# Kernel optimization log

Hardware: AMD Instinct MI355X
Metric: run time of the kernel (lower is better)

## Reference

```python
import jax, jax.numpy as jnp
import numpy as np
from jax import lax


def linear_recurrence(decays, impulses):
    """s[t] = decays[t]*s[t-1] + impulses[t], s[-1]=0, via associative scan over axis 0."""
    def comb(e1, e2):
        a1, b1 = e1
        a2, b2 = e2
        return a2 * a1, a2 * b1 + b2
    return lax.associative_scan(comb, (decays, impulses), axis=0)[1]


def setup_inputs() -> dict:
    key = jax.random.key(0)
    ks = jax.random.split(key, 6)
    b, T, d = 16, 1024, 128
    n, m, k = 64, 128, 16
    x = jax.random.normal(ks[0], (b, T, d), jnp.float32)
    R = jax.random.normal(ks[1], (d, k), jnp.float32)               # fixed projection
    theta = jax.random.uniform(ks[2], (k, n // 2), jnp.float32, -np.pi, np.pi)  # eig angles
    C = jax.random.uniform(ks[3], (k, m, n), jnp.float32, -1e-6, 1e-6) / n
    D = jax.random.uniform(ks[4], (k, m), jnp.float32, -1e-3, 1e-3)
    Do = jax.random.uniform(ks[5], (m,), jnp.float32, -1e-7, 1e-7)
    return {"x": x, "R": R, "theta": theta, "C": C, "D": D, "Do": Do}


def _ldstack(x, R, theta, C, D, Do, Delta=2, standard=True):
    c64 = jnp.complex64
    b, T, d = x.shape
    k, half = theta.shape
    n = 2 * half
    m = C.shape[1]
    # (b,T,d) -> (T,b,d) complex, project d -> k
    xc = jnp.transpose(x, (1, 0, 2)).astype(c64) @ R.astype(c64)  # (T,b,k)
    # unitary eigenvalues: lnλ = i*[θ, -θ]
    lnlam = (1j * jnp.concatenate([theta, -theta], axis=1)).astype(c64)  # (k,n)
    lam = jnp.exp(lnlam)
    # B' coefficients (log-space product over eigenvalue ratios, diag excluded)
    eye = jnp.eye(n, dtype=bool)
    ratios = jnp.where(eye[None], 0.0, lam[:, :, None] / lam[:, None, :])  # (k,n,n)
    B = jnp.exp(-jnp.sum(jnp.log(1.0 - ratios), axis=1))                    # (k,n)
    # C' coefficients: C'[k,j,m] = sum_i C[k,m,i] * λ[k,j]^{-(n-i)}
    powers = (n - jnp.arange(1, n + 1)).astype(c64)           # (n,) = [n-1,...,0]
    U = jnp.exp(-powers[None, :, None] * lnlam[:, None, :])   # (k,i,j)
    Cp = jnp.einsum('kmi,kij->kjm', C.astype(c64), U)         # (k,n,m)
    Dc = D.astype(c64)
    Doc = Do.astype(c64)

    alpha = None
    y = None
    for _ in range(Delta):
        Bx = (xc[..., None] * B).reshape(T, b, k * n)          # (T,b,k*n)
        if alpha is None:
            al = jnp.broadcast_to(lam.reshape(1, 1, k * n), (T, b, k * n))
        else:
            al = (alpha * lam).reshape(T, b, k * n)
        if standard:
            z = jnp.zeros((1, b, k * n), c64)
            al = jnp.concatenate([z, al[:-1]], axis=0)
            Bx = jnp.concatenate([z, Bx[:-1]], axis=0)
        s = linear_recurrence(al, Bx).reshape(T, b, k, n)      # (T,b,k,n)
        y = (jnp.einsum('tbkn,knm->tbkm', s, Cp)
             + xc[..., None] * Dc[None, None]
             + Doc)                                            # (T,b,k,m)
        ls = lam[None, None] * s
        alpha = (1.0 / jnp.sqrt(1.0 + jnp.abs(ls) ** 2)).astype(c64)  # recipsq
    y = jnp.mean(y, axis=2).real                               # (T,b,m)
    return jnp.transpose(y, (1, 0, 2))                         # (b,T,m)


def reference(x, R, theta, C, D, Do):
    return _ldstack(x, R, theta, C, D, Do, Delta=2, standard=True)
```

## Files before the change

kernel.cpp:

```cpp
#include <hip/hip_runtime.h>
#include <math.h>

#define TLEN 1024
#define BSZ  16
#define DIN  128
#define KP   16
#define NEIG 64
#define MOUT 128
#define CHUNK_T 256
#define NCHUNK  4

static constexpr size_t XCQ_OFF = 0;
static constexpr size_t LAM_OFF = 262144;
static constexpr size_t BQ_OFF  = 264192;
static constexpr size_t CP_OFF  = 266240;
static constexpr size_t ST_OFF  = 528384;
static constexpr size_t S2_OFF  = 593920;
static constexpr size_t P_OFF   = 8982528;

__device__ __forceinline__ float f32cos(float x) { return (float)cos((double)x); }
__device__ __forceinline__ float f32sin(float x) { return (float)sin((double)x); }

__device__ __forceinline__ float2 cdiv32(float ar, float ai, float cr, float ci) {
  float2 o;
  if (fabsf(ci) <= fabsf(cr)) {
    float rat = __fdiv_rn(ci, cr);
    float scl = __fdiv_rn(1.0f, __fadd_rn(cr, __fmul_rn(ci, rat)));
    o.x = __fmul_rn(__fadd_rn(ar, __fmul_rn(ai, rat)), scl);
    o.y = __fmul_rn(__fsub_rn(ai, __fmul_rn(ar, rat)), scl);
  } else {
    float rat = __fdiv_rn(cr, ci);
    float scl = __fdiv_rn(1.0f, __fadd_rn(ci, __fmul_rn(cr, rat)));
    o.x = __fmul_rn(__fadd_rn(__fmul_rn(ar, rat), ai), scl);
    o.y = __fmul_rn(__fsub_rn(__fmul_rn(ai, rat), ar), scl);
  }
  return o;
}

__global__ __launch_bounds__(256) void k_lam_B(const float* __restrict__ theta,
                        float2* __restrict__ lam, float2* __restrict__ Bq) {
  __shared__ float2 terms[4][64];
  int wid  = threadIdx.x >> 6;
  int lane = threadIdx.x & 63;
  int idx = blockIdx.x * 4 + wid;
  int k = idx >> 6, j = idx & 63;
  float thj = (j < 32) ? theta[k * 32 + j] : -theta[k * 32 + (j - 32)];
  float ljr = f32cos(thj), lji = f32sin(thj);
  float2 tm = make_float2(0.f, 0.f);
  if (lane != j) {
    int i = lane;
    float thi = (i < 32) ? theta[k * 32 + i] : -theta[k * 32 + (i - 32)];
    float lir = f32cos(thi), lii = f32sin(thi);
    float2 r = cdiv32(lir, lii, ljr, lji);
    float tr = __fsub_rn(1.0f, r.x);
    float ti = __fsub_rn(0.0f, r.y);
    double h = sqrt((double)tr * tr + (double)ti * ti);
    tm.x = (float)log(h);
    tm.y = (float)atan2((double)ti, (double)tr);
  }
  terms[wid][lane] = tm;
  __syncthreads();
  if (lane == 0) {
    lam[idx] = make_float2(ljr, lji);
    float sr = 0.f, si = 0.f;
    for (int i = 0; i < NEIG; ++i) {
      sr = __fadd_rn(sr, terms[wid][i].x);
      si = __fadd_rn(si, terms[wid][i].y);
    }
    float er = (float)exp((double)(-sr));
    float cc = f32cos(-si), ss = f32sin(-si);
    Bq[idx] = make_float2(__fmul_rn(er, cc), __fmul_rn(er, ss));
  }
}

__global__ __launch_bounds__(128) void k_Cp(const float* __restrict__ theta,
                     const float* __restrict__ C, float2* __restrict__ Cp) {
  __shared__ float2 sU[64];
  __shared__ float  sC[128][65];
  int tid = threadIdx.x;
  int kj = blockIdx.x;
  int j = kj & 63, k = kj >> 6;
  float lnim = (j < 32) ? theta[k * 32 + j] : -theta[k * 32 + (j - 32)];
  if (tid < 64) {
    int i = tid;
    float p = (float)(63 - i);
    float ph = -__fmul_rn(p, lnim);
    sU[i] = make_float2(f32cos(ph), f32sin(ph));
  }
  const float* Ck = C + ((size_t)k << 13);
  for (int e = tid; e < 128 * 64; e += 128) {
    sC[e >> 6][e & 63] = Ck[e];
  }
  __syncthreads();
  int m = tid;
  float ar = 0.f, ai = 0.f;
  #pragma unroll 8
  for (int i = 0; i < NEIG; ++i) {
    float Cv = sC[m][i];
    float2 U = sU[i];
    ar = __fadd_rn(ar, __fmul_rn(Cv, U.x));
    ai = __fadd_rn(ai, __fmul_rn(Cv, U.y));
  }
  Cp[(size_t)(k * 64 + j) * MOUT + m] = make_float2(ar, ai);
}

__global__ __launch_bounds__(256) void k_xc(const float* __restrict__ x,
                     const float* __restrict__ R, float* __restrict__ xcq) {
  __shared__ float sX[16][132];
  __shared__ float sR[128][16];
  int tid = threadIdx.x;
  int rBase = blockIdx.x * 16;
  for (int e = tid; e < DIN * KP; e += 256) sR[e >> 4][e & 15] = R[e];
  #pragma unroll
  for (int it = 0; it < 2; ++it) {
    int e = tid + it * 256;
    int row = e >> 5, q = e & 31;
    int g = rBase + row;
    int t = g >> 4, b = g & 15;
    float4 v = *(const float4*)(x + ((size_t)b * TLEN + t) * DIN + q * 4);
    *(float4*)&sX[row][q * 4] = v;
  }
  __syncthreads();
  int r = tid >> 4, k = tid & 15;
  double acc = 0.0;
  #pragma unroll 16
  for (int d = 0; d < DIN; ++d)
    acc = fma((double)sX[r][d], (double)sR[d][k], acc);
  xcq[(size_t)(rBase + r) * KP + k] = (float)acc;
}

__global__ __launch_bounds__(64) void k_scan(const float2* __restrict__ lam,
                        const float2* __restrict__ Bq,
                        const float* __restrict__ xcq,
                        float2* __restrict__ S2,
                        float* __restrict__ state, int c) {
  __shared__ float sXq[CHUNK_T];
  int j = threadIdx.x;
  int chain = blockIdx.x;
  int b = chain >> 4, k = chain & 15;
  int mode = k * 64 + j;
  int t0 = c * CHUNK_T;
  int tlBeg = (c == 0) ? 1 : 0;
  for (int i = j; i < CHUNK_T; i += 64) {
    int g = t0 + tlBeg - 1 + i;
    sXq[i] = xcq[(size_t)g * (BSZ * KP) + b * KP + k];
  }
  __syncthreads();
  float lr = lam[mode].x, li = lam[mode].y;
  float Br = Bq[mode].x,  Bi = Bq[mode].y;
  float* st = state + (size_t)(chain * 64 + j) * 4;
  float s1r, s1i, s2r, s2i;
  if (c == 0) { s1r = s1i = s2r = s2i = 0.f; }
  else        { s1r = st[0]; s1i = st[1]; s2r = st[2]; s2i = st[3]; }
  if (c == 0)
    S2[(size_t)(0 * BSZ + b) * 1024 + mode] = make_float2(s2r, s2i);

  int tl = tlBeg;
  for (; tl + 8 <= CHUNK_T; tl += 8) {
    float als[8];
    #pragma unroll
    for (int u = 0; u < 8; ++u) {
      float xq = sXq[tl - tlBeg + u];
      float lsr = __fsub_rn(__fmul_rn(lr, s1r), __fmul_rn(li, s1i));
      float lsi = __fadd_rn(__fmul_rn(lr, s1i), __fmul_rn(li, s1r));
      float h  = (float)sqrt((double)lsr * lsr + (double)lsi * lsi);
      als[u] = __fdiv_rn(1.0f, __fsqrt_rn(__fadd_rn(1.0f, __fmul_rn(h, h))));
      float bxr = __fmul_rn(xq, Br), bxi = __fmul_rn(xq, Bi);
      s1r = __fadd_rn(lsr, bxr);
      s1i = __fadd_rn(lsi, bxi);
    }
    #pragma unroll
    for (int u = 0; u < 8; ++u) {
      float xq = sXq[tl - tlBeg + u];
      float al = als[u];
      float bxr = __fmul_rn(xq, Br), bxi = __fmul_rn(xq, Bi);
      float a2r = __fmul_rn(al, lr), a2i = __fmul_rn(al, li);
      float t2r = __fsub_rn(__fmul_rn(a2r, s2r), __fmul_rn(a2i, s2i));
      float t2i = __fadd_rn(__fmul_rn(a2r, s2i), __fmul_rn(a2i, s2r));
      s2r = __fadd_rn(t2r, bxr);
      s2i = __fadd_rn(t2i, bxi);
      S2[(size_t)((tl + u) * BSZ + b) * 1024 + mode] = make_float2(s2r, s2i);
    }
  }
  for (; tl < CHUNK_T; ++tl) {
    float xq = sXq[tl - tlBeg];
    float lsr = __fsub_rn(__fmul_rn(lr, s1r), __fmul_rn(li, s1i));
    float lsi = __fadd_rn(__fmul_rn(lr, s1i), __fmul_rn(li, s1r));
    float h  = (float)sqrt((double)lsr * lsr + (double)lsi * lsi);
    float al = __fdiv_rn(1.0f, __fsqrt_rn(__fadd_rn(1.0f, __fmul_rn(h, h))));
    float bxr = __fmul_rn(xq, Br), bxi = __fmul_rn(xq, Bi);
    float a2r = __fmul_rn(al, lr), a2i = __fmul_rn(al, li);
    float t2r = __fsub_rn(__fmul_rn(a2r, s2r), __fmul_rn(a2i, s2i));
    float t2i = __fadd_rn(__fmul_rn(a2r, s2i), __fmul_rn(a2i, s2r));
    s2r = __fadd_rn(t2r, bxr);
    s2i = __fadd_rn(t2i, bxi);
    s1r = __fadd_rn(lsr, bxr);
    s1i = __fadd_rn(lsi, bxi);
    S2[(size_t)(tl * BSZ + b) * 1024 + mode] = make_float2(s2r, s2i);
  }
  st[0] = s1r; st[1] = s1i; st[2] = s2r; st[3] = s2i;
}

__global__ __launch_bounds__(256) void k_y(const float2* __restrict__ S2,
                     const float2* __restrict__ Cp, const float* __restrict__ xcq,
                     const float* __restrict__ D, const float* __restrict__ Dov,
                     float* __restrict__ P, int c) {
  __shared__ float2 sS2t[16][65];
  __shared__ float2 sCp[16][130];
  int tid = threadIdx.x;
  int kidx = blockIdx.x >> 6;
  int rt   = blockIdx.x & 63;
  int rowBase = rt * 64;
  int rg = tid & 15;
  int cg = tid >> 4;
  int c0 = cg * 8;
  float acc[4][8];
  #pragma unroll
  for (int jj = 0; jj < 4; ++jj)
    #pragma unroll
    for (int q = 0; q < 8; ++q) acc[jj][q] = 0.f;

  #pragma unroll 1
  for (int nh = 0; nh < 4; ++nh) {
    __syncthreads();
    #pragma unroll
    for (int it = 0; it < 2; ++it) {
      int e = tid + it * 256;
      int n2 = (e & 7) * 2;
      int row = e >> 3;
      float4 v = *(const float4*)(S2 + (size_t)(rowBase + row) * 1024
                                     + kidx * 64 + nh * 16 + n2);
      sS2t[n2][row]     = make_float2(v.x, v.y);
      sS2t[n2 + 1][row] = make_float2(v.z, v.w);
    }
    #pragma unroll
    for (int it = 0; it < 4; ++it) {
      int e = tid + it * 256;
      int col2 = (e & 63) * 2;
      int n = e >> 6;
      float4 v = *(const float4*)(Cp + (size_t)(kidx * 64 + nh * 16 + n) * MOUT + col2);
      *(float4*)&sCp[n][col2] = v;
    }
    __syncthreads();
    #pragma unroll 4
    for (int n = 0; n < 16; ++n) {
      float2 a[4];
      #pragma unroll
      for (int jj = 0; jj < 4; ++jj) a[jj] = sS2t[n][rg + jj * 16];
      float4 w[4];
      #pragma unroll
      for (int q = 0; q < 4; ++q) w[q] = *(const float4*)&sCp[n][c0 + q * 2];
      float cx[8] = {w[0].x, w[0].z, w[1].x, w[1].z, w[2].x, w[2].z, w[3].x, w[3].z};
      float cy[8] = {w[0].y, w[0].w, w[1].y, w[1].w, w[2].y, w[2].w, w[3].y, w[3].w};
      #pragma unroll
      for (int jj = 0; jj < 4; ++jj)
        #pragma unroll
        for (int q = 0; q < 8; ++q)
          acc[jj][q] = __fadd_rn(acc[jj][q],
              __fsub_rn(__fmul_rn(a[jj].x, cx[q]), __fmul_rn(a[jj].y, cy[q])));
    }
  }
  float dv[8], ovv[8];
  *(float4*)&dv[0]  = *(const float4*)(D + kidx * MOUT + c0);
  *(float4*)&dv[4]  = *(const float4*)(D + kidx * MOUT + c0 + 4);
  *(float4*)&ovv[0] = *(const float4*)(Dov + c0);
  *(float4*)&ovv[4] = *(const float4*)(Dov + c0 + 4);
  #pragma unroll
  for (int jj = 0; jj < 4; ++jj) {
    int row = rowBase + rg + jj * 16;
    float xv = xcq[(size_t)(c * 4096 + row) * KP + kidx];
    float res[8];
    #pragma unroll
    for (int q = 0; q < 8; ++q)
      res[q] = __fadd_rn(__fadd_rn(acc[jj][q], __fmul_rn(xv, dv[q])), ovv[q]);
    float* pp = P + ((size_t)kidx * 4096 + row) * MOUT + c0;
    *(float4*)pp       = make_float4(res[0], res[1], res[2], res[3]);
    *(float4*)(pp + 4) = make_float4(res[4], res[5], res[6], res[7]);
  }
}

__global__ __launch_bounds__(256) void k_combine(const float* __restrict__ P,
                     float* __restrict__ out, int c) {
  int idx = blockIdx.x * 256 + threadIdx.x;
  int r  = idx >> 5;
  int m4 = (idx & 31) * 4;
  float4 s = *(const float4*)(P + (size_t)r * MOUT + m4);
  #pragma unroll
  for (int k = 1; k < KP; ++k) {
    float4 p = *(const float4*)(P + ((size_t)k * 4096 + r) * MOUT + m4);
    s.x = __fadd_rn(s.x, p.x);
    s.y = __fadd_rn(s.y, p.y);
    s.z = __fadd_rn(s.z, p.z);
    s.w = __fadd_rn(s.w, p.w);
  }
  int rg = c * 4096 + r;
  int t = rg >> 4, b = rg & 15;
  float4 res;
  res.x = __fdiv_rn(s.x, 16.0f);
  res.y = __fdiv_rn(s.y, 16.0f);
  res.z = __fdiv_rn(s.z, 16.0f);
  res.w = __fdiv_rn(s.w, 16.0f);
  *(float4*)(out + ((size_t)b * TLEN + t) * MOUT + m4) = res;
}

extern "C" void kernel_launch(void* const* d_in, const int* in_sizes, int n_in,
                              void* d_out, int out_size, void* d_ws, size_t ws_size,
                              hipStream_t stream) {
  const float* x     = (const float*)d_in[0];
  const float* R     = (const float*)d_in[1];
  const float* theta = (const float*)d_in[2];
  const float* C     = (const float*)d_in[3];
  const float* D     = (const float*)d_in[4];
  const float* Do    = (const float*)d_in[5];
  float* out = (float*)d_out;
  float* ws  = (float*)d_ws;
  float*  xcq = ws + XCQ_OFF;
  float2* lam = (float2*)(ws + LAM_OFF);
  float2* Bq  = (float2*)(ws + BQ_OFF);
  float2* Cp  = (float2*)(ws + CP_OFF);
  float*  st  = ws + ST_OFF;
  float2* S2  = (float2*)(ws + S2_OFF);
  float*  P   = ws + P_OFF;

  hipLaunchKernelGGL(k_lam_B, dim3(256),  dim3(256), 0, stream, theta, lam, Bq);
  hipLaunchKernelGGL(k_Cp,    dim3(1024), dim3(128), 0, stream, theta, C, Cp);
  hipLaunchKernelGGL(k_xc,    dim3(1024), dim3(256), 0, stream, x, R, xcq);
  for (int c = 0; c < NCHUNK; ++c) {
    hipLaunchKernelGGL(k_scan,    dim3(256),  dim3(64),  0, stream, lam, Bq, xcq, S2, st, c);
    hipLaunchKernelGGL(k_y,       dim3(1024), dim3(256), 0, stream, S2, Cp, xcq, D, Do, P, c);
    hipLaunchKernelGGL(k_combine, dim3(512),  dim3(256), 0, stream, P, out, c);
  }
}
```

Baseline: 372.1 us.

## Fuse scan, projection and combine into one software-pipelined kernel per chunk

Replaces the three per-chunk kernels with one fused kernel launched per pipeline step. Each launch runs the scan for chunk L, the C' projection for chunk L-1 and the k-reduction for chunk L-2 in separate block ranges, using double-buffered S2 and P. Chunks shrink to 128 timesteps, so there are more, smaller stages. The aim is to overlap the latency-bound serial scan, which uses only 64 blocks, with the throughput-bound GEMM and reduction, and to cut launch count. The cost is more pipeline steps and a larger branchy kernel whose register use is set by its heaviest path.

```diff
diff --git a/kernel.cpp b/kernel.cpp
--- a/kernel.cpp
+++ b/kernel.cpp
@@ -7,8 +7,9 @@
 #define KP   16
 #define NEIG 64
 #define MOUT 128
-#define CHUNK_T 256
-#define NCHUNK  4
+#define CHUNK_T 128
+#define NCHUNK  8
+#define CROWS   2048
 
 static constexpr size_t XCQ_OFF = 0;
 static constexpr size_t LAM_OFF = 262144;
@@ -129,178 +130,187 @@
   xcq[(size_t)(rBase + r) * KP + k] = (float)acc;
 }
 
-__global__ __launch_bounds__(64) void k_scan(const float2* __restrict__ lam,
-                        const float2* __restrict__ Bq,
-                        const float* __restrict__ xcq,
-                        float2* __restrict__ S2,
-                        float* __restrict__ state, int c) {
-  __shared__ float sXq[CHUNK_T];
-  int j = threadIdx.x;
-  int chain = blockIdx.x;
-  int b = chain >> 4, k = chain & 15;
-  int mode = k * 64 + j;
-  int t0 = c * CHUNK_T;
-  int tlBeg = (c == 0) ? 1 : 0;
-  for (int i = j; i < CHUNK_T; i += 64) {
-    int g = t0 + tlBeg - 1 + i;
-    sXq[i] = xcq[(size_t)g * (BSZ * KP) + b * KP + k];
-  }
-  __syncthreads();
-  float lr = lam[mode].x, li = lam[mode].y;
-  float Br = Bq[mode].x,  Bi = Bq[mode].y;
-  float* st = state + (size_t)(chain * 64 + j) * 4;
-  float s1r, s1i, s2r, s2i;
-  if (c == 0) { s1r = s1i = s2r = s2i = 0.f; }
-  else        { s1r = st[0]; s1i = st[1]; s2r = st[2]; s2i = st[3]; }
-  if (c == 0)
-    S2[(size_t)(0 * BSZ + b) * 1024 + mode] = make_float2(s2r, s2i);
-
-  int tl = tlBeg;
-  for (; tl + 8 <= CHUNK_T; tl += 8) {
-    float als[8];
+__global__ __launch_bounds__(256) void k_fused(int L,
+                     const float2* __restrict__ lam, const float2* __restrict__ Bq,
+                     const float* __restrict__ xcq, const float2* __restrict__ Cp,
+                     const float* __restrict__ D, const float* __restrict__ Dov,
+                     float2* __restrict__ S2all, float* __restrict__ Pall,
+                     float* __restrict__ state, float* __restrict__ out) {
+  __shared__ float2 sS2t[16][65];
+  __shared__ float2 sCp[16][66];
+  __shared__ float  sXq[4][132];
+  int bid = blockIdx.x;
+  int tid = threadIdx.x;
+  int nKy   = (L >= 1 && L <= 8) ? 1024 : 0;
+  int nScan = (L < 8) ? 64 : 0;
+
+  if (bid < nKy) {
+    int cK = L - 1;
+    const float2* S2 = S2all + (size_t)(cK & 1) * 2097152;
+    float* P = Pall + (size_t)(cK & 1) * 4194304;
+    int kidx = bid >> 6;
+    int rem  = bid & 63;
+    int rowBase = (rem >> 1) * 64;
+    int colBase = (rem & 1) * 64;
+    int rg = tid & 15;
+    int cg = tid >> 4;
+    float acc[4][4];
     #pragma unroll
-    for (int u = 0; u < 8; ++u) {
-      float xq = sXq[tl - tlBeg + u];
+    for (int jj = 0; jj < 4; ++jj)
+      #pragma unroll
+      for (int q = 0; q < 4; ++q) acc[jj][q] = 0.f;
+
+    #pragma unroll 1
+    for (int nh = 0; nh < 4; ++nh) {
+      __syncthreads();
+      #pragma unroll
+      for (int it = 0; it < 2; ++it) {
+        int e = tid + it * 256;
+        int n2 = (e & 7) * 2;
+        int row = e >> 3;
+        float4 v = *(const float4*)(S2 + (size_t)(rowBase + row) * 1024
+                                       + kidx * 64 + nh * 16 + n2);
+        sS2t[n2][row]     = make_float2(v.x, v.y);
+        sS2t[n2 + 1][row] = make_float2(v.z, v.w);
+      }
+      #pragma unroll
+      for (int it = 0; it < 2; ++it) {
+        int e = tid + it * 256;
+        int col2 = (e & 31) * 2;
+        int n = e >> 5;
+        float4 v = *(const float4*)(Cp + (size_t)(kidx * 64 + nh * 16 + n) * MOUT
+                                       + colBase + col2);
+        *(float4*)&sCp[n][col2] = v;
+      }
+      __syncthreads();
+      #pragma unroll 4
+      for (int n = 0; n < 16; ++n) {
+        float2 a[4];
+        #pragma unroll
+        for (int jj = 0; jj < 4; ++jj) a[jj] = sS2t[n][rg + jj * 16];
+        float4 w0 = *(const float4*)&sCp[n][cg * 4];
+        float4 w1 = *(const float4*)&sCp[n][cg * 4 + 2];
+        float cx[4] = {w0.x, w0.z, w1.x, w1.z};
+        float cy[4] = {w0.y, w0.w, w1.y, w1.w};
+        #pragma unroll
+        for (int jj = 0; jj < 4; ++jj)
+          #pragma unroll
+          for (int q = 0; q < 4; ++q)
+            acc[jj][q] = __fadd_rn(acc[jj][q],
+                __fsub_rn(__fmul_rn(a[jj].x, cx[q]), __fmul_rn(a[jj].y, cy[q])));
+      }
+    }
+    float4 d4 = *(const float4*)(D + kidx * MOUT + colBase + cg * 4);
+    float4 o4 = *(const float4*)(Dov + colBase + cg * 4);
+    float dv[4] = {d4.x, d4.y, d4.z, d4.w};
+    float ov[4] = {o4.x, o4.y, o4.z, o4.w};
+    #pragma unroll
+    for (int jj = 0; jj < 4; ++jj) {
+      int row = rowBase + rg + jj * 16;
+      float xv = xcq[(size_t)(cK * CROWS + row) * KP + kidx];
+      float res[4];
+      #pragma unroll
+      for (int q = 0; q < 4; ++q)
+        res[q] = __fadd_rn(__fadd_rn(acc[jj][q], __fmul_rn(xv, dv[q])), ov[q]);
+      *(float4*)(P + ((size_t)kidx * CROWS + row) * MOUT + colBase + cg * 4)
+          = make_float4(res[0], res[1], res[2], res[3]);
+    }
+  } else if (bid < nKy + nScan) {
+    int cS = L;
+    float2* S2 = S2all + (size_t)(cS & 1) * 2097152;
+    int w = tid >> 6, j = tid & 63;
+    int chain = (bid - nKy) * 4 + w;
+    int b = chain >> 4;
+    int mode = (chain & 15) * 64 + j;
+    int t0 = cS * CHUNK_T;
+    int tlBeg = (cS == 0) ? 1 : 0;
+    for (int i = j; i < CHUNK_T; i += 64) {
+      int g = t0 + tlBeg - 1 + i;
+      sXq[w][i] = xcq[(size_t)g * 256 + chain];
+    }
+    __syncthreads();
+    float lr = lam[mode + (chain & 15) * 0].x, li = lam[mode].y;
+    lr = lam[mode].x;
+    float Br = Bq[mode].x, Bi = Bq[mode].y;
+    float* st = state + (size_t)(chain * 64 + j) * 4;
+    float s1r, s1i, s2r, s2i;
+    if (cS == 0) { s1r = s1i = s2r = s2i = 0.f; }
+    else         { s1r = st[0]; s1i = st[1]; s2r = st[2]; s2i = st[3]; }
+    if (cS == 0)
+      S2[(size_t)(0 * BSZ + b) * 1024 + mode] = make_float2(s2r, s2i);
+
+    int tl = tlBeg;
+    for (; tl + 8 <= CHUNK_T; tl += 8) {
+      float als[8];
+      #pragma unroll
+      for (int u = 0; u < 8; ++u) {
+        float xq = sXq[w][tl - tlBeg + u];
+        float lsr = __fsub_rn(__fmul_rn(lr, s1r), __fmul_rn(li, s1i));
+        float lsi = __fadd_rn(__fmul_rn(lr, s1i), __fmul_rn(li, s1r));
+        float h  = (float)sqrt((double)lsr * lsr + (double)lsi * lsi);
+        als[u] = __fdiv_rn(1.0f, __fsqrt_rn(__fadd_rn(1.0f, __fmul_rn(h, h))));
+        float bxr = __fmul_rn(xq, Br), bxi = __fmul_rn(xq, Bi);
+        s1r = __fadd_rn(lsr, bxr);
+        s1i = __fadd_rn(lsi, bxi);
+      }
+      #pragma unroll
+      for (int u = 0; u < 8; ++u) {
+        float xq = sXq[w][tl - tlBeg + u];
+        float al = als[u];
+        float bxr = __fmul_rn(xq, Br), bxi = __fmul_rn(xq, Bi);
+        float a2r = __fmul_rn(al, lr), a2i = __fmul_rn(al, li);
+        float t2r = __fsub_rn(__fmul_rn(a2r, s2r), __fmul_rn(a2i, s2i));
+        float t2i = __fadd_rn(__fmul_rn(a2r, s2i), __fmul_rn(a2i, s2r));
+        s2r = __fadd_rn(t2r, bxr);
+        s2i = __fadd_rn(t2i, bxi);
+        S2[(size_t)((tl + u) * BSZ + b) * 1024 + mode] = make_float2(s2r, s2i);
+      }
+    }
+    for (; tl < CHUNK_T; ++tl) {
+      float xq = sXq[w][tl - tlBeg];
       float lsr = __fsub_rn(__fmul_rn(lr, s1r), __fmul_rn(li, s1i));
       float lsi = __fadd_rn(__fmul_rn(lr, s1i), __fmul_rn(li, s1r));
       float h  = (float)sqrt((double)lsr * lsr + (double)lsi * lsi);
-      als[u] = __fdiv_rn(1.0f, __fsqrt_rn(__fadd_rn(1.0f, __fmul_rn(h, h))));
-      float bxr = __fmul_rn(xq, Br), bxi = __fmul_rn(xq, Bi);
-      s1r = __fadd_rn(lsr, bxr);
-      s1i = __fadd_rn(lsi, bxi);
-    }
-    #pragma unroll
-    for (int u = 0; u < 8; ++u) {
-      float xq = sXq[tl - tlBeg + u];
-      float al = als[u];
+      float al = __fdiv_rn(1.0f, __fsqrt_rn(__fadd_rn(1.0f, __fmul_rn(h, h))));
       float bxr = __fmul_rn(xq, Br), bxi = __fmul_rn(xq, Bi);
       float a2r = __fmul_rn(al, lr), a2i = __fmul_rn(al, li);
       float t2r = __fsub_rn(__fmul_rn(a2r, s2r), __fmul_rn(a2i, s2i));
       float t2i = __fadd_rn(__fmul_rn(a2r, s2i), __fmul_rn(a2i, s2r));
       s2r = __fadd_rn(t2r, bxr);
       s2i = __fadd_rn(t2i, bxi);
-      S2[(size_t)((tl + u) * BSZ + b) * 1024 + mode] = make_float2(s2r, s2i);
-    }
-  }
-  for (; tl < CHUNK_T; ++tl) {
-    float xq = sXq[tl - tlBeg];
-    float lsr = __fsub_rn(__fmul_rn(lr, s1r), __fmul_rn(li, s1i));
-    float lsi = __fadd_rn(__fmul_rn(lr, s1i), __fmul_rn(li, s1r));
-    float h  = (float)sqrt((double)lsr * lsr + (double)lsi * lsi);
-    float al = __fdiv_rn(1.0f, __fsqrt_rn(__fadd_rn(1.0f, __fmul_rn(h, h))));
-    float bxr = __fmul_rn(xq, Br), bxi = __fmul_rn(xq, Bi);
-    float a2r = __fmul_rn(al, lr), a2i = __fmul_rn(al, li);
-    float t2r = __fsub_rn(__fmul_rn(a2r, s2r), __fmul_rn(a2i, s2i));
-    float t2i = __fadd_rn(__fmul_rn(a2r, s2i), __fmul_rn(a2i, s2r));
-    s2r = __fadd_rn(t2r, bxr);
-    s2i = __fadd_rn(t2i, bxi);
-    s1r = __fadd_rn(lsr, bxr);
-    s1i = __fadd_rn(lsi, bxi);
-    S2[(size_t)(tl * BSZ + b) * 1024 + mode] = make_float2(s2r, s2i);
-  }
-  st[0] = s1r; st[1] = s1i; st[2] = s2r; st[3] = s2i;
-}
-
-__global__ __launch_bounds__(256) void k_y(const float2* __restrict__ S2,
-                     const float2* __restrict__ Cp, const float* __restrict__ xcq,
-                     const float* __restrict__ D, const float* __restrict__ Dov,
-                     float* __restrict__ P, int c) {
-  __shared__ float2 sS2t[16][65];
-  __shared__ float2 sCp[16][130];
-  int tid = threadIdx.x;
-  int kidx = blockIdx.x >> 6;
-  int rt   = blockIdx.x & 63;
-  int rowBase = rt * 64;
-  int rg = tid & 15;
-  int cg = tid >> 4;
-  int c0 = cg * 8;
-  float acc[4][8];
-  #pragma unroll
-  for (int jj = 0; jj < 4; ++jj)
-    #pragma unroll
-    for (int q = 0; q < 8; ++q) acc[jj][q] = 0.f;
-
-  #pragma unroll 1
-  for (int nh = 0; nh < 4; ++nh) {
-    __syncthreads();
+      s1r = __fadd_rn(lsr, bxr);
+      s1i = __fadd_rn(lsi, bxi);
+      S2[(size_t)(tl * BSZ + b) * 1024 + mode] = make_float2(s2r, s2i);
+    }
+    st[0] = s1r; st[1] = s1i; st[2] = s2r; st[3] = s2i;
+  } else {
+    int cC = L - 2;
+    const float* P = Pall + (size_t)(cC & 1) * 4194304;
+    int cb = bid - nKy - nScan;
     #pragma unroll
     for (int it = 0; it < 2; ++it) {
-      int e = tid + it * 256;
-      int n2 = (e & 7) * 2;
-      int row = e >> 3;
-      float4 v = *(const float4*)(S2 + (size_t)(rowBase + row) * 1024
-                                     + kidx * 64 + nh * 16 + n2);
-      sS2t[n2][row]     = make_float2(v.x, v.y);
-      sS2t[n2 + 1][row] = make_float2(v.z, v.w);
-    }
-    #pragma unroll
-    for (int it = 0; it < 4; ++it) {
-      int e = tid + it * 256;
-      int col2 = (e & 63) * 2;
-      int n = e >> 6;
-      float4 v = *(const float4*)(Cp + (size_t)(kidx * 64 + nh * 16 + n) * MOUT + col2);
-      *(float4*)&sCp[n][col2] = v;
-    }
-    __syncthreads();
-    #pragma unroll 4
-    for (int n = 0; n < 16; ++n) {
-      float2 a[4];
-      #pragma unroll
-      for (int jj = 0; jj < 4; ++jj) a[jj] = sS2t[n][rg + jj * 16];
-      float4 w[4];
-      #pragma unroll
-      for (int q = 0; q < 4; ++q) w[q] = *(const float4*)&sCp[n][c0 + q * 2];
-      float cx[8] = {w[0].x, w[0].z, w[1].x, w[1].z, w[2].x, w[2].z, w[3].x, w[3].z};
-      float cy[8] = {w[0].y, w[0].w, w[1].y, w[1].w, w[2].y, w[2].w, w[3].y, w[3].w};
-      #pragma unroll
-      for (int jj = 0; jj < 4; ++jj)
-        #pragma unroll
-        for (int q = 0; q < 8; ++q)
-          acc[jj][q] = __fadd_rn(acc[jj][q],
-              __fsub_rn(__fmul_rn(a[jj].x, cx[q]), __fmul_rn(a[jj].y, cy[q])));
-    }
-  }
-  float dv[8], ovv[8];
-  *(float4*)&dv[0]  = *(const float4*)(D + kidx * MOUT + c0);
-  *(float4*)&dv[4]  = *(const float4*)(D + kidx * MOUT + c0 + 4);
-  *(float4*)&ovv[0] = *(const float4*)(Dov + c0);
-  *(float4*)&ovv[4] = *(const float4*)(Dov + c0 + 4);
-  #pragma unroll
-  for (int jj = 0; jj < 4; ++jj) {
-    int row = rowBase + rg + jj * 16;
-    float xv = xcq[(size_t)(c * 4096 + row) * KP + kidx];
-    float res[8];
-    #pragma unroll
-    for (int q = 0; q < 8; ++q)
-      res[q] = __fadd_rn(__fadd_rn(acc[jj][q], __fmul_rn(xv, dv[q])), ovv[q]);
-    float* pp = P + ((size_t)kidx * 4096 + row) * MOUT + c0;
-    *(float4*)pp       = make_float4(res[0], res[1], res[2], res[3]);
-    *(float4*)(pp + 4) = make_float4(res[4], res[5], res[6], res[7]);
-  }
-}
-
-__global__ __launch_bounds__(256) void k_combine(const float* __restrict__ P,
-                     float* __restrict__ out, int c) {
-  int idx = blockIdx.x * 256 + threadIdx.x;
-  int r  = idx >> 5;
-  int m4 = (idx & 31) * 4;
-  float4 s = *(const float4*)(P + (size_t)r * MOUT + m4);
-  #pragma unroll
-  for (int k = 1; k < KP; ++k) {
-    float4 p = *(const float4*)(P + ((size_t)k * 4096 + r) * MOUT + m4);
-    s.x = __fadd_rn(s.x, p.x);
-    s.y = __fadd_rn(s.y, p.y);
-    s.z = __fadd_rn(s.z, p.z);
-    s.w = __fadd_rn(s.w, p.w);
-  }
-  int rg = c * 4096 + r;
-  int t = rg >> 4, b = rg & 15;
-  float4 res;
-  res.x = __fdiv_rn(s.x, 16.0f);
-  res.y = __fdiv_rn(s.y, 16.0f);
-  res.z = __fdiv_rn(s.z, 16.0f);
-  res.w = __fdiv_rn(s.w, 16.0f);
-  *(float4*)(out + ((size_t)b * TLEN + t) * MOUT + m4) = res;
+      int e = cb * 512 + tid + it * 256;
+      int r  = e >> 5;
+      int m4 = (e & 31) * 4;
+      float4 s = *(const float4*)(P + (size_t)r * MOUT + m4);
+      #pragma unroll
+      for (int k = 1; k < KP; ++k) {
+        float4 p = *(const float4*)(P + ((size_t)k * CROWS + r) * MOUT + m4);
+        s.x = __fadd_rn(s.x, p.x);
+        s.y = __fadd_rn(s.y, p.y);
+        s.z = __fadd_rn(s.z, p.z);
+        s.w = __fadd_rn(s.w, p.w);
+      }
+      int gr = cC * CROWS + r;
+      int t = gr >> 4, b = gr & 15;
+      float4 res;
+      res.x = __fdiv_rn(s.x, 16.0f);
+      res.y = __fdiv_rn(s.y, 16.0f);
+      res.z = __fdiv_rn(s.z, 16.0f);
+      res.w = __fdiv_rn(s.w, 16.0f);
+      *(float4*)(out + ((size_t)b * TLEN + t) * MOUT + m4) = res;
+    }
+  }
 }
 
 extern "C" void kernel_launch(void* const* d_in, const int* in_sizes, int n_in,
@@ -325,9 +335,11 @@
   hipLaunchKernelGGL(k_lam_B, dim3(256),  dim3(256), 0, stream, theta, lam, Bq);
   hipLaunchKernelGGL(k_Cp,    dim3(1024), dim3(128), 0, stream, theta, C, Cp);
   hipLaunchKernelGGL(k_xc,    dim3(1024), dim3(256), 0, stream, x, R, xcq);
-  for (int c = 0; c < NCHUNK; ++c) {
-    hipLaunchKernelGGL(k_scan,    dim3(256),  dim3(64),  0, stream, lam, Bq, xcq, S2, st, c);
-    hipLaunchKernelGGL(k_y,       dim3(1024), dim3(256), 0, stream, S2, Cp, xcq, D, Do, P, c);
-    hipLaunchKernelGGL(k_combine, dim3(512),  dim3(256), 0, stream, P, out, c);
-  }
-}
+  for (int L = 0; L <= NCHUNK + 1; ++L) {
+    int nKy   = (L >= 1 && L <= NCHUNK) ? 1024 : 0;
+    int nScan = (L < NCHUNK) ? 64 : 0;
+    int nComb = (L >= 2) ? 128 : 0;
+    hipLaunchKernelGGL(k_fused, dim3(nKy + nScan + nComb), dim3(256), 0, stream,
+                       L, lam, Bq, xcq, Cp, D, Do, S2, P, st, out);
+  }
+}
```

New measurement: 345.4 us. -7.2%, faster.
